# Optimization experiments

Hardware: AMD Instinct MI355X
Metric: run time of the kernel (lower is better)

Reference implementation:

```python
import jax, jax.numpy as jnp
import numpy as np

NEG_SLOPE = 0.2
BN_EPS = 1e-5

def lrelu(x):
    return jnp.where(x >= 0, x, NEG_SLOPE * x)

def setup_inputs() -> dict:
    key = jax.random.key(0)
    ks = jax.random.split(key, 12)
    B, V, D = 256, 16, 512
    s = lambda fan_in: 1.0 / np.sqrt(fan_in)
    return {
        "F": jax.random.normal(ks[0], (B, V, D), dtype=jnp.float32),
        # Relation MLP: Linear(1024,512) x3 (stored as (in,out))
        "W1": jax.random.uniform(ks[1], (2 * D, D), jnp.float32, -s(2 * D), s(2 * D)),
        "b1": jax.random.uniform(ks[2], (D,), jnp.float32, -s(2 * D), s(2 * D)),
        "W2": jax.random.uniform(ks[3], (D, D), jnp.float32, -s(D), s(D)),
        "b2": jax.random.uniform(ks[4], (D,), jnp.float32, -s(D), s(D)),
        "W3": jax.random.uniform(ks[5], (D, D), jnp.float32, -s(D), s(D)),
        "b3": jax.random.uniform(ks[6], (D,), jnp.float32, -s(D), s(D)),
        # Fusion: Linear(1024,512) + BatchNorm1d(512)
        "Wf": jax.random.uniform(ks[7], (2 * D, D), jnp.float32, -s(2 * D), s(2 * D)),
        "bf": jax.random.uniform(ks[8], (D,), jnp.float32, -s(2 * D), s(2 * D)),
        "gamma": jnp.ones((D,), jnp.float32),
        "beta": jnp.zeros((D,), jnp.float32),
    }

def reference(F, W1, b1, W2, b2, W3, b3, Wf, bf, gamma, beta):
    B, V, D = F.shape
    # All-pairs broadcast + concat -> (B, V, V, 2D)
    F_i = jnp.broadcast_to(F[:, :, None, :], (B, V, V, D))
    F_j = jnp.broadcast_to(F[:, None, :, :], (B, V, V, D))
    M = jnp.concatenate([F_i, F_j], axis=-1)
    # 3-layer Relation MLP with LeakyReLU(0.2)
    h = lrelu(M @ W1 + b1)
    h = lrelu(h @ W2 + b2)
    h = lrelu(h @ W3 + b3)
    # Sum over neighbor axis (dim -2) -> (B, V, D)
    Msum = jnp.sum(h, axis=-2)
    # Fusion: concat, Linear, BatchNorm1d (training-mode batch stats), LeakyReLU
    X = jnp.concatenate([F, Msum], axis=-1).reshape(-1, 2 * D)  # (B*V, 2D)
    y = X @ Wf + bf
    mean = jnp.mean(y, axis=0)
    var = jnp.mean(jnp.square(y - mean), axis=0)  # biased var (torch BN)
    yn = (y - mean) * jax.lax.rsqrt(var + BN_EPS) * gamma + beta
    return lrelu(yn).reshape(B, V, D)
```

## Files before the change

kernel.cpp:

```cpp
#include <hip/hip_runtime.h>

using f32x4  = __attribute__((ext_vector_type(4))) float;
using bf16x8 = __attribute__((ext_vector_type(8))) __bf16;

static constexpr int DD = 512;
static constexpr int NTOK = 4096;

__device__ __forceinline__ float bf2f(unsigned short u) {
  unsigned int v = ((unsigned int)u) << 16;
  return __builtin_bit_cast(float, v);
}
__device__ __forceinline__ float bflo(unsigned int u) {
  return __builtin_bit_cast(float, u << 16);
}
__device__ __forceinline__ float bfhi(unsigned int u) {
  return __builtin_bit_cast(float, u & 0xffff0000u);
}
__device__ __forceinline__ unsigned short f2bf(float f) {
  unsigned int u = __builtin_bit_cast(unsigned int, f);
  unsigned int r = u + 0x7fffu + ((u >> 16) & 1u);
  return (unsigned short)(r >> 16);
}
__device__ __forceinline__ float lrelu(float v) { return v >= 0.f ? v : 0.2f * v; }


__global__ __launch_bounds__(256) void k_prep(const float* __restrict__ F,
                                              const float* __restrict__ W1,
                                              const float* __restrict__ W2,
                                              const float* __restrict__ W3,
                                              const float* __restrict__ Wf,
                                              unsigned short* __restrict__ XP,
                                              unsigned short* __restrict__ W1P,
                                              unsigned short* __restrict__ W2P,
                                              unsigned short* __restrict__ W3P,
                                              unsigned short* __restrict__ WfP,
                                              float* __restrict__ sums) {
  const int bid = blockIdx.x, tid = threadIdx.x;
  if (bid < 8192) {
    int idx = (bid << 8) + tid;
    int t = idx >> 9, c = idx & 511;
    XP[((t >> 4) * 32 + (c >> 5)) * 512 + ((c >> 3) & 3) * 128 + (t & 15) * 8 + (c & 7)] = f2bf(F[idx]);
  } else if (bid < 10240) {
    int idx = ((bid - 8192) << 8) + tid;
    int k = idx >> 10, n = idx & 1023;
    float v = W1[(n < 512 ? k : 512 + k) * 512 + (n & 511)];
    W1P[((n >> 4) * 16 + (k >> 5)) * 512 + ((k >> 3) & 3) * 128 + (n & 15) * 8 + (k & 7)] = f2bf(v);
  } else if (bid < 11264) {
    int idx = ((bid - 10240) << 8) + tid;
    int k = idx >> 9, n = idx & 511;
    W2P[((n >> 4) * 16 + (k >> 5)) * 512 + ((k >> 3) & 3) * 128 + (n & 15) * 8 + (k & 7)] = f2bf(W2[idx]);
  } else if (bid < 12288) {
    int idx = ((bid - 11264) << 8) + tid;
    int k = idx >> 9, n = idx & 511;
    W3P[((n >> 4) * 16 + (k >> 5)) * 512 + ((k >> 3) & 3) * 128 + (n & 15) * 8 + (k & 7)] = f2bf(W3[idx]);
  } else if (bid < 14336) {
    int idx = ((bid - 12288) << 8) + tid;
    int k = idx >> 9, n = idx & 511;
    WfP[((n >> 4) * 32 + (k >> 5)) * 512 + ((k >> 3) & 3) * 128 + (n & 15) * 8 + (k & 7)] = f2bf(Wf[idx]);
  } else {
    reinterpret_cast<float4*>(sums)[tid] = float4{0.f, 0.f, 0.f, 0.f};
  }
}

__global__ __launch_bounds__(512) void k_gemm_ac(const unsigned short* __restrict__ XP,
                                                 const unsigned short* __restrict__ W1P,
                                                 unsigned short* __restrict__ ACP) {
  const int tid = threadIdx.x, lane = tid & 63, wid = tid >> 6;
  const int wm = wid >> 2, wn = wid & 3;
  const int l15 = lane & 15;
  const int bx = blockIdx.x, by = blockIdx.y;

  f32x4 acc[2][4];
#pragma unroll
  for (int mt = 0; mt < 2; ++mt)
#pragma unroll
    for (int nt = 0; nt < 4; ++nt) acc[mt][nt] = f32x4{0.f, 0.f, 0.f, 0.f};

  bf16x8 ca[2], cb[4], na[2], nb[4];
  auto ldA = [&](bf16x8 (&d)[2], int ks) {
#pragma unroll
    for (int mt = 0; mt < 2; ++mt)
      d[mt] = *reinterpret_cast<const bf16x8*>(XP + (((bx * 4 + wm * 2 + mt) * 32 + ks) << 9) + lane * 8);
  };
  auto ldB = [&](bf16x8 (&d)[4], int ks) {
#pragma unroll
    for (int nt = 0; nt < 4; ++nt)
      d[nt] = *reinterpret_cast<const bf16x8*>(W1P + ((((by * 16 + wn * 4 + nt) * 16) + ks) << 9) + lane * 8);
  };

  ldA(ca, 0); ldB(cb, 0);
  for (int ks = 0; ks < 16; ++ks) {
    int kn = (ks + 1) & 15;
    ldA(na, kn); ldB(nb, kn);
    __builtin_amdgcn_s_setprio(1);
#pragma unroll
    for (int mt = 0; mt < 2; ++mt)
#pragma unroll
      for (int nt = 0; nt < 4; ++nt)
        acc[mt][nt] = __builtin_amdgcn_mfma_f32_16x16x32_bf16(ca[mt], cb[nt], acc[mt][nt], 0, 0, 0);
    __builtin_amdgcn_s_setprio(0);
#pragma unroll
    for (int q = 0; q < 2; ++q) ca[q] = na[q];
#pragma unroll
    for (int q = 0; q < 4; ++q) cb[q] = nb[q];
  }
#pragma unroll
  for (int mt = 0; mt < 2; ++mt)
#pragma unroll
    for (int nt = 0; nt < 4; ++nt) {
      int col = by * 256 + wn * 64 + nt * 16 + l15;
      int panel = bx * 4 + wm * 2 + mt;
#pragma unroll
      for (int r = 0; r < 4; ++r) {
        int rowi = (lane >> 4) * 4 + r;
        ACP[(panel * 32 + (col >> 5)) * 512 + ((col >> 3) & 3) * 128 + rowi * 8 + (col & 7)] = f2bf(acc[mt][nt][r]);
      }
    }
}

__global__ __launch_bounds__(512, 2) void k_relation(const unsigned short* __restrict__ ACP,
                                                     const unsigned short* __restrict__ W2P,
                                                     const unsigned short* __restrict__ W3P,
                                                     const float* __restrict__ b1,
                                                     const float* __restrict__ b2,
                                                     const float* __restrict__ b3,
                                                     unsigned short* __restrict__ XP) {
  __shared__ unsigned short lds[65536];
  const int tid = threadIdx.x;
  const int b = blockIdx.x >> 1, half = blockIdx.x & 1;

  {
    const int r = tid >> 2;
    const int il = r >> 4, j = r & 15;
    const int rowA = half * 8 + il;
    const int kq = tid & 3;
#pragma unroll
    for (int ks = 0; ks < 16; ++ks) {
      const int c = ks * 32 + kq * 8;
      uint4 av = *reinterpret_cast<const uint4*>(ACP + ((b * 32 + ks) << 9) + kq * 128 + rowA * 8);
      uint4 cv = *reinterpret_cast<const uint4*>(ACP + ((b * 32 + 16 + ks) << 9) + kq * 128 + j * 8);
      float4 bv0 = *reinterpret_cast<const float4*>(b1 + c);
      float4 bv1 = *reinterpret_cast<const float4*>(b1 + c + 4);
      unsigned int au[4] = {av.x, av.y, av.z, av.w};
      unsigned int cu[4] = {cv.x, cv.y, cv.z, cv.w};
      float bb[8] = {bv0.x, bv0.y, bv0.z, bv0.w, bv1.x, bv1.y, bv1.z, bv1.w};
      unsigned int ou[4];
#pragma unroll
      for (int q = 0; q < 4; ++q) {
        float v0 = lrelu(bflo(au[q]) + bflo(cu[q]) + bb[2 * q]);
        float v1 = lrelu(bf2f((unsigned short)(au[q] >> 16)) +
                         bf2f((unsigned short)(cu[q] >> 16)) + bb[2 * q + 1]);
        ou[q] = ((unsigned int)f2bf(v1) << 16) | (unsigned int)f2bf(v0);
      }
      uint4 o; o.x = ou[0]; o.y = ou[1]; o.z = ou[2]; o.w = ou[3];
      *reinterpret_cast<uint4*>(lds + (((r >> 4) * 16 + ks) << 9) + kq * 128 + (r & 15) * 8) = o;
    }
  }
  __syncthreads();

  const int lane = tid & 63, wid = tid >> 6;
  const int l15 = lane & 15;
  const int fg = wid >> 1;
  const int rg = wid & 1;

  f32x4 acc[8][4];
  bf16x8 ca[8], na[8], cb[4];

  auto ldA = [&](bf16x8 (&d)[8], const unsigned short* __restrict__ Wp, int ks) {
#pragma unroll
    for (int mt = 0; mt < 8; ++mt)
      d[mt] = *reinterpret_cast<const bf16x8*>(Wp + (((fg * 8 + mt) * 16 + ks) << 9) + lane * 8);
  };
  auto ldB = [&](bf16x8 (&d)[4], int ks) {
#pragma unroll
    for (int nt = 0; nt < 4; ++nt)
      d[nt] = *reinterpret_cast<const bf16x8*>(lds + ((((rg * 4 + nt) * 16) + ks) << 9) + lane * 8);
  };
  auto store_h = [&](f32x4 (&a)[8][4], const float* __restrict__ bias) {
#pragma unroll
    for (int mt = 0; mt < 8; ++mt) {
      float4 bv = *reinterpret_cast<const float4*>(bias + fg * 128 + mt * 16 + (lane >> 4) * 4);
      int ks2 = fg * 4 + (mt >> 1);
      int kq2 = (mt & 1) * 2 + ((lane >> 4) >> 1);
#pragma unroll
      for (int nt = 0; nt < 4; ++nt) {
        unsigned int w0 = f2bf(lrelu(a[mt][nt][0] + bv.x));
        unsigned int w1 = f2bf(lrelu(a[mt][nt][1] + bv.y));
        unsigned int w2 = f2bf(lrelu(a[mt][nt][2] + bv.z));
        unsigned int w3 = f2bf(lrelu(a[mt][nt][3] + bv.w));
        uint2 val; val.x = (w1 << 16) | w0; val.y = (w3 << 16) | w2;
        int off = (((rg * 4 + nt) * 16 + ks2) << 9) + kq2 * 128 + l15 * 8 + ((lane >> 4) & 1) * 4;
        *reinterpret_cast<uint2*>(lds + off) = val;
      }
    }
  };
  auto layer = [&](const unsigned short* __restrict__ Wp) {
#pragma unroll
    for (int mt = 0; mt < 8; ++mt)
#pragma unroll
      for (int nt = 0; nt < 4; ++nt) acc[mt][nt] = f32x4{0.f, 0.f, 0.f, 0.f};
    ldA(ca, Wp, 0);
    for (int ks = 0; ks < 16; ++ks) {
      ldA(na, Wp, (ks + 1) & 15);
      ldB(cb, ks);
      __builtin_amdgcn_s_setprio(1);
#pragma unroll
      for (int mt = 0; mt < 8; ++mt)
#pragma unroll
        for (int nt = 0; nt < 4; ++nt)
          acc[mt][nt] = __builtin_amdgcn_mfma_f32_16x16x32_bf16(ca[mt], cb[nt], acc[mt][nt], 0, 0, 0);
      __builtin_amdgcn_s_setprio(0);
#pragma unroll
      for (int q = 0; q < 8; ++q) ca[q] = na[q];
    }
  };

  layer(W2P);
  __syncthreads();
  store_h(acc, b2);
  __syncthreads();

  layer(W3P);
  __syncthreads();
  store_h(acc, b3);
  __syncthreads();

  {
    const int t = wid;
    const int fb = lane;
    const int ks = fb >> 2, kq = fb & 3;
    const unsigned short* base = lds + ((t * 16 + ks) << 9) + kq * 128;
    float s[8] = {0.f, 0.f, 0.f, 0.f, 0.f, 0.f, 0.f, 0.f};
    for (int it = 0; it < 16; ++it) {
      int j = (it + lane) & 15;
      uint4 v = *reinterpret_cast<const uint4*>(base + j * 8);
      s[0] += bflo(v.x); s[1] += bfhi(v.x);
      s[2] += bflo(v.y); s[3] += bfhi(v.y);
      s[4] += bflo(v.z); s[5] += bfhi(v.z);
      s[6] += bflo(v.w); s[7] += bfhi(v.w);
    }
    uint4 o;
    o.x = ((unsigned int)f2bf(s[1]) << 16) | f2bf(s[0]);
    o.y = ((unsigned int)f2bf(s[3]) << 16) | f2bf(s[2]);
    o.z = ((unsigned int)f2bf(s[5]) << 16) | f2bf(s[4]);
    o.w = ((unsigned int)f2bf(s[7]) << 16) | f2bf(s[6]);
    int tg15 = half * 8 + t;
    *reinterpret_cast<uint4*>(XP + ((b * 32 + 16 + ks) << 9) + kq * 128 + tg15 * 8) = o;
  }
}

__global__ __launch_bounds__(512) void k_fusion(const unsigned short* __restrict__ XP,
                                                const unsigned short* __restrict__ WfP,
                                                const float* __restrict__ bfv,
                                                float* __restrict__ y,
                                                float* __restrict__ sums,
                                                float* __restrict__ sumsq) {
  const int tid = threadIdx.x, lane = tid & 63, wid = tid >> 6;
  const int wm = wid >> 2, wn = wid & 3;
  const int l15 = lane & 15;
  const int bx = blockIdx.x, by = blockIdx.y;
  const int rowbase = bx * 64 + wm * 32;
  const int colbase = by * 128 + wn * 32;

  f32x4 acc[2][2];
#pragma unroll
  for (int mt = 0; mt < 2; ++mt)
#pragma unroll
    for (int nt = 0; nt < 2; ++nt) acc[mt][nt] = f32x4{0.f, 0.f, 0.f, 0.f};

  bf16x8 ca[2], cb[2], na[2], nb[2];
  auto ldA = [&](bf16x8 (&d)[2], int ks) {
#pragma unroll
    for (int mt = 0; mt < 2; ++mt)
      d[mt] = *reinterpret_cast<const bf16x8*>(XP + (((bx * 4 + wm * 2 + mt) * 32 + ks) << 9) + lane * 8);
  };
  auto ldB = [&](bf16x8 (&d)[2], int ks) {
#pragma unroll
    for (int nt = 0; nt < 2; ++nt)
      d[nt] = *reinterpret_cast<const bf16x8*>(WfP + (((by * 8 + wn * 2 + nt) * 32 + ks) << 9) + lane * 8);
  };

  ldA(ca, 0); ldB(cb, 0);
  for (int ks = 0; ks < 32; ++ks) {
    int kn = (ks + 1) & 31;
    ldA(na, kn); ldB(nb, kn);
    __builtin_amdgcn_s_setprio(1);
#pragma unroll
    for (int mt = 0; mt < 2; ++mt)
#pragma unroll
      for (int nt = 0; nt < 2; ++nt)
        acc[mt][nt] = __builtin_amdgcn_mfma_f32_16x16x32_bf16(ca[mt], cb[nt], acc[mt][nt], 0, 0, 0);
    __builtin_amdgcn_s_setprio(0);
#pragma unroll
    for (int q = 0; q < 2; ++q) { ca[q] = na[q]; cb[q] = nb[q]; }
  }

  float s[2] = {0.f, 0.f}, q2[2] = {0.f, 0.f};
#pragma unroll
  for (int nt = 0; nt < 2; ++nt) {
    int col = colbase + nt * 16 + l15;
    float bias = bfv[col];
#pragma unroll
    for (int mt = 0; mt < 2; ++mt)
#pragma unroll
      for (int r = 0; r < 4; ++r) {
        int row = rowbase + mt * 16 + (lane >> 4) * 4 + r;
        float v = acc[mt][nt][r] + bias;
        y[row * DD + col] = v;
        s[nt] += v; q2[nt] += v * v;
      }
  }
#pragma unroll
  for (int nt = 0; nt < 2; ++nt) {
    s[nt] += __shfl_xor(s[nt], 16);  s[nt] += __shfl_xor(s[nt], 32);
    q2[nt] += __shfl_xor(q2[nt], 16); q2[nt] += __shfl_xor(q2[nt], 32);
    if (lane < 16) {
      int col = colbase + nt * 16 + l15;
      atomicAdd(&sums[col], s[nt]);
      atomicAdd(&sumsq[col], q2[nt]);
    }
  }
}

__global__ __launch_bounds__(256) void k_bnapply(const float* __restrict__ y,
                                                 const float* __restrict__ sums,
                                                 const float* __restrict__ sumsq,
                                                 const float* __restrict__ gamma,
                                                 const float* __restrict__ beta,
                                                 float* __restrict__ out) {
  int idx = blockIdx.x * 256 + threadIdx.x;
  if (idx >= NTOK * DD) return;
  int c = idx & 511;
  float mean = sums[c] * (1.0f / 4096.0f);
  float var = sumsq[c] * (1.0f / 4096.0f) - mean * mean;
  float rstd = rsqrtf(var + 1e-5f);
  float v = (y[idx] - mean) * rstd * gamma[c] + beta[c];
  out[idx] = lrelu(v);
}

extern "C" void kernel_launch(void* const* d_in, const int* in_sizes, int n_in,
                              void* d_out, int out_size, void* d_ws, size_t ws_size,
                              hipStream_t stream) {
  const float* F   = (const float*)d_in[0];
  const float* W1  = (const float*)d_in[1];
  const float* b1  = (const float*)d_in[2];
  const float* W2  = (const float*)d_in[3];
  const float* b2  = (const float*)d_in[4];
  const float* W3  = (const float*)d_in[5];
  const float* b3  = (const float*)d_in[6];
  const float* Wf  = (const float*)d_in[7];
  const float* bfv = (const float*)d_in[8];
  const float* gamma = (const float*)d_in[9];
  const float* beta  = (const float*)d_in[10];
  float* out = (float*)d_out;

  char* ws = (char*)d_ws;
  unsigned short* XP  = (unsigned short*)(ws);
  unsigned short* ACP = (unsigned short*)(ws + (8u << 20));
  unsigned short* W1P = (unsigned short*)(ws + (16u << 20));
  unsigned short* W2P = (unsigned short*)(ws + (17u << 20));
  unsigned short* W3P = (unsigned short*)(ws + (17u << 20) + (512u << 10));
  unsigned short* WfP = (unsigned short*)(ws + (18u << 20));
  float* y            = (float*)(ws + (19u << 20));
  float* sums         = (float*)(ws + (27u << 20));
  float* sumsq        = sums + 512;

  k_prep<<<14337, 256, 0, stream>>>(F, W1, W2, W3, Wf, XP, W1P, W2P, W3P, WfP, sums);
  k_gemm_ac<<<dim3(64, 4), 512, 0, stream>>>(XP, W1P, ACP);
  k_relation<<<512, 512, 0, stream>>>(ACP, W2P, W3P, b1, b2, b3, XP);
  k_fusion<<<dim3(64, 4), 512, 0, stream>>>(XP, WfP, bfv, y, sums, sumsq);
  k_bnapply<<<(NTOK * DD + 255) / 256, 256, 0, stream>>>(y, sums, sumsq, gamma, beta, out);
}
```

Measured before the change: 126.2 us.

## Double relation kernel threads to 1024 with repacked W2/W3 and smaller per-warp tiles

Relaunches the relation-MLP kernel with 1024 threads (16 waves) per block in place of 512, so each wave owns a 64x64 output tile (4x4 MFMAs) rather than 128x64. W2/W3 are repacked so that each wave's weight slice for one k-step is contiguous, with a two-stage register double buffer for A. The LDS addressing is rewritten in bytes and the neighbour-sum reads are staggered to reduce bank conflicts. Each wave holds fewer registers and there are more waves to hide latency, but the launch-bounds change drops the 2-blocks-per-CU hint and every wave now reloads the shared activation B tiles.

```diff
diff --git a/kernel.cpp b/kernel.cpp
--- a/kernel.cpp
+++ b/kernel.cpp
@@ -48,11 +48,13 @@
   } else if (bid < 11264) {
     int idx = ((bid - 10240) << 8) + tid;
     int k = idx >> 9, n = idx & 511;
-    W2P[((n >> 4) * 16 + (k >> 5)) * 512 + ((k >> 3) & 3) * 128 + (n & 15) * 8 + (k & 7)] = f2bf(W2[idx]);
+    int off = (((n >> 6) * 16 + (k >> 5)) * 4 + ((n >> 4) & 3)) * 512 + ((k >> 3) & 3) * 128 + (n & 15) * 8 + (k & 7);
+    W2P[off] = f2bf(W2[idx]);
   } else if (bid < 12288) {
     int idx = ((bid - 11264) << 8) + tid;
     int k = idx >> 9, n = idx & 511;
-    W3P[((n >> 4) * 16 + (k >> 5)) * 512 + ((k >> 3) & 3) * 128 + (n & 15) * 8 + (k & 7)] = f2bf(W3[idx]);
+    int off = (((n >> 6) * 16 + (k >> 5)) * 4 + ((n >> 4) & 3)) * 512 + ((k >> 3) & 3) * 128 + (n & 15) * 8 + (k & 7);
+    W3P[off] = f2bf(W3[idx]);
   } else if (bid < 14336) {
     int idx = ((bid - 12288) << 8) + tid;
     int k = idx >> 9, n = idx & 511;
@@ -118,24 +120,27 @@
     }
 }
 
-__global__ __launch_bounds__(512, 2) void k_relation(const unsigned short* __restrict__ ACP,
-                                                     const unsigned short* __restrict__ W2P,
-                                                     const unsigned short* __restrict__ W3P,
-                                                     const float* __restrict__ b1,
-                                                     const float* __restrict__ b2,
-                                                     const float* __restrict__ b3,
-                                                     unsigned short* __restrict__ XP) {
+__global__ __launch_bounds__(1024) void k_relation(const unsigned short* __restrict__ ACP,
+                                                   const unsigned short* __restrict__ W2P,
+                                                   const unsigned short* __restrict__ W3P,
+                                                   const float* __restrict__ b1,
+                                                   const float* __restrict__ b2,
+                                                   const float* __restrict__ b3,
+                                                   unsigned short* __restrict__ XP) {
   __shared__ unsigned short lds[65536];
+  char* ldsb = reinterpret_cast<char*>(lds);
   const int tid = threadIdx.x;
   const int b = blockIdx.x >> 1, half = blockIdx.x & 1;
 
   {
-    const int r = tid >> 2;
+    const int r = tid >> 3;
+    const int kh = (tid >> 2) & 1;
+    const int kq = tid & 3;
     const int il = r >> 4, j = r & 15;
     const int rowA = half * 8 + il;
-    const int kq = tid & 3;
-#pragma unroll
-    for (int ks = 0; ks < 16; ++ks) {
+#pragma unroll
+    for (int kk = 0; kk < 8; ++kk) {
+      const int ks = kh * 8 + kk;
       const int c = ks * 32 + kq * 8;
       uint4 av = *reinterpret_cast<const uint4*>(ACP + ((b * 32 + ks) << 9) + kq * 128 + rowA * 8);
       uint4 cv = *reinterpret_cast<const uint4*>(ACP + ((b * 32 + 16 + ks) << 9) + kq * 128 + j * 8);
@@ -148,12 +153,11 @@
 #pragma unroll
       for (int q = 0; q < 4; ++q) {
         float v0 = lrelu(bflo(au[q]) + bflo(cu[q]) + bb[2 * q]);
-        float v1 = lrelu(bf2f((unsigned short)(au[q] >> 16)) +
-                         bf2f((unsigned short)(cu[q] >> 16)) + bb[2 * q + 1]);
+        float v1 = lrelu(bfhi(au[q]) + bfhi(cu[q]) + bb[2 * q + 1]);
         ou[q] = ((unsigned int)f2bf(v1) << 16) | (unsigned int)f2bf(v0);
       }
       uint4 o; o.x = ou[0]; o.y = ou[1]; o.z = ou[2]; o.w = ou[3];
-      *reinterpret_cast<uint4*>(lds + (((r >> 4) * 16 + ks) << 9) + kq * 128 + (r & 15) * 8) = o;
+      *reinterpret_cast<uint4*>(ldsb + ((r >> 4) * 16 + ks) * 1024 + kq * 256 + (r & 15) * 16) = o;
     }
   }
   __syncthreads();
@@ -163,77 +167,76 @@
   const int fg = wid >> 1;
   const int rg = wid & 1;
 
-  f32x4 acc[8][4];
-  bf16x8 ca[8], na[8], cb[4];
-
-  auto ldA = [&](bf16x8 (&d)[8], const unsigned short* __restrict__ Wp, int ks) {
-#pragma unroll
-    for (int mt = 0; mt < 8; ++mt)
-      d[mt] = *reinterpret_cast<const bf16x8*>(Wp + (((fg * 8 + mt) * 16 + ks) << 9) + lane * 8);
-  };
-  auto ldB = [&](bf16x8 (&d)[4], int ks) {
-#pragma unroll
-    for (int nt = 0; nt < 4; ++nt)
-      d[nt] = *reinterpret_cast<const bf16x8*>(lds + ((((rg * 4 + nt) * 16) + ks) << 9) + lane * 8);
-  };
-  auto store_h = [&](f32x4 (&a)[8][4], const float* __restrict__ bias) {
-#pragma unroll
-    for (int mt = 0; mt < 8; ++mt) {
-      float4 bv = *reinterpret_cast<const float4*>(bias + fg * 128 + mt * 16 + (lane >> 4) * 4);
-      int ks2 = fg * 4 + (mt >> 1);
-      int kq2 = (mt & 1) * 2 + ((lane >> 4) >> 1);
+  const unsigned short* w2base = W2P + (fg << 15) + lane * 8;
+  const unsigned short* w3base = W3P + (fg << 15) + lane * 8;
+  const char* lrd = ldsb + rg * 65536 + lane * 16;
+  char* lwr = ldsb + rg * 65536 + fg * 2048 + ((lane >> 5) & 1) * 256 + ((lane >> 4) & 1) * 8 + l15 * 16;
+
+  f32x4 acc[4][4];
+  bf16x8 a[2][4], cb[4];
+
+  auto layer = [&](const unsigned short* __restrict__ wb) {
+#pragma unroll
+    for (int mt = 0; mt < 4; ++mt)
+#pragma unroll
+      for (int nt = 0; nt < 4; ++nt) acc[mt][nt] = f32x4{0.f, 0.f, 0.f, 0.f};
+#pragma unroll
+    for (int mt = 0; mt < 4; ++mt)
+      a[0][mt] = *reinterpret_cast<const bf16x8*>(wb + mt * 512);
+#pragma unroll
+    for (int ks = 0; ks < 16; ++ks) {
+      const int cur = ks & 1, nxt = cur ^ 1;
+      const int ksn = (ks + 1) & 15;
+#pragma unroll
+      for (int mt = 0; mt < 4; ++mt)
+        a[nxt][mt] = *reinterpret_cast<const bf16x8*>(wb + ksn * 2048 + mt * 512);
+#pragma unroll
+      for (int nt = 0; nt < 4; ++nt)
+        cb[nt] = *reinterpret_cast<const bf16x8*>(lrd + nt * 16384 + ks * 1024);
+      __builtin_amdgcn_s_setprio(1);
+#pragma unroll
+      for (int mt = 0; mt < 4; ++mt)
+#pragma unroll
+        for (int nt = 0; nt < 4; ++nt)
+          acc[mt][nt] = __builtin_amdgcn_mfma_f32_16x16x32_bf16(a[cur][mt], cb[nt], acc[mt][nt], 0, 0, 0);
+      __builtin_amdgcn_s_setprio(0);
+    }
+  };
+
+  auto store_h = [&](const float* __restrict__ bias) {
+#pragma unroll
+    for (int mt = 0; mt < 4; ++mt) {
+      float4 bv = *reinterpret_cast<const float4*>(bias + fg * 64 + mt * 16 + ((lane >> 4) & 3) * 4);
 #pragma unroll
       for (int nt = 0; nt < 4; ++nt) {
-        unsigned int w0 = f2bf(lrelu(a[mt][nt][0] + bv.x));
-        unsigned int w1 = f2bf(lrelu(a[mt][nt][1] + bv.y));
-        unsigned int w2 = f2bf(lrelu(a[mt][nt][2] + bv.z));
-        unsigned int w3 = f2bf(lrelu(a[mt][nt][3] + bv.w));
+        unsigned int w0 = f2bf(lrelu(acc[mt][nt][0] + bv.x));
+        unsigned int w1 = f2bf(lrelu(acc[mt][nt][1] + bv.y));
+        unsigned int w2 = f2bf(lrelu(acc[mt][nt][2] + bv.z));
+        unsigned int w3 = f2bf(lrelu(acc[mt][nt][3] + bv.w));
         uint2 val; val.x = (w1 << 16) | w0; val.y = (w3 << 16) | w2;
-        int off = (((rg * 4 + nt) * 16 + ks2) << 9) + kq2 * 128 + l15 * 8 + ((lane >> 4) & 1) * 4;
-        *reinterpret_cast<uint2*>(lds + off) = val;
+        *reinterpret_cast<uint2*>(lwr + nt * 16384 + (mt >> 1) * 1024 + (mt & 1) * 512) = val;
       }
     }
   };
-  auto layer = [&](const unsigned short* __restrict__ Wp) {
-#pragma unroll
-    for (int mt = 0; mt < 8; ++mt)
-#pragma unroll
-      for (int nt = 0; nt < 4; ++nt) acc[mt][nt] = f32x4{0.f, 0.f, 0.f, 0.f};
-    ldA(ca, Wp, 0);
-    for (int ks = 0; ks < 16; ++ks) {
-      ldA(na, Wp, (ks + 1) & 15);
-      ldB(cb, ks);
-      __builtin_amdgcn_s_setprio(1);
-#pragma unroll
-      for (int mt = 0; mt < 8; ++mt)
-#pragma unroll
-        for (int nt = 0; nt < 4; ++nt)
-          acc[mt][nt] = __builtin_amdgcn_mfma_f32_16x16x32_bf16(ca[mt], cb[nt], acc[mt][nt], 0, 0, 0);
-      __builtin_amdgcn_s_setprio(0);
-#pragma unroll
-      for (int q = 0; q < 8; ++q) ca[q] = na[q];
-    }
-  };
-
-  layer(W2P);
-  __syncthreads();
-  store_h(acc, b2);
-  __syncthreads();
-
-  layer(W3P);
-  __syncthreads();
-  store_h(acc, b3);
-  __syncthreads();
-
-  {
+
+  layer(w2base);
+  __syncthreads();
+  store_h(b2);
+  __syncthreads();
+  layer(w3base);
+  __syncthreads();
+  store_h(b3);
+  __syncthreads();
+
+  if (wid < 8) {
     const int t = wid;
-    const int fb = lane;
-    const int ks = fb >> 2, kq = fb & 3;
-    const unsigned short* base = lds + ((t * 16 + ks) << 9) + kq * 128;
+    const int ks = lane >> 2, kq = lane & 3;
+    const char* base = ldsb + (t * 16 + ks) * 1024 + kq * 256;
     float s[8] = {0.f, 0.f, 0.f, 0.f, 0.f, 0.f, 0.f, 0.f};
+#pragma unroll
     for (int it = 0; it < 16; ++it) {
-      int j = (it + lane) & 15;
-      uint4 v = *reinterpret_cast<const uint4*>(base + j * 8);
+      int j = (it + lane + (lane >> 3)) & 15;
+      uint4 v = *reinterpret_cast<const uint4*>(base + j * 16);
       s[0] += bflo(v.x); s[1] += bfhi(v.x);
       s[2] += bflo(v.y); s[3] += bfhi(v.y);
       s[4] += bflo(v.z); s[5] += bfhi(v.z);
@@ -367,7 +370,7 @@
 
   k_prep<<<14337, 256, 0, stream>>>(F, W1, W2, W3, Wf, XP, W1P, W2P, W3P, WfP, sums);
   k_gemm_ac<<<dim3(64, 4), 512, 0, stream>>>(XP, W1P, ACP);
-  k_relation<<<512, 512, 0, stream>>>(ACP, W2P, W3P, b1, b2, b3, XP);
+  k_relation<<<512, 1024, 0, stream>>>(ACP, W2P, W3P, b1, b2, b3, XP);
   k_fusion<<<dim3(64, 4), 512, 0, stream>>>(XP, WfP, bfv, y, sums, sumsq);
   k_bnapply<<<(NTOK * DD + 255) / 256, 256, 0, stream>>>(y, sums, sumsq, gamma, beta, out);
 }
```

Result: no change. 124.3 us (-1.5%).
